# Optimization experiments

Hardware: AMD Instinct MI355X
Metric: run time of the kernel (lower is better)

## Reference

```python
import jax, jax.numpy as jnp
import numpy as np

N, D_IN, D_H, D_A, K = 131072, 768, 128, 32, 64
BN_EPS = 1e-5

def setup_inputs() -> dict:
    key = jax.random.key(0)
    ks = jax.random.split(key, 16)
    def lin(k, fan_in, shape):
        return (jax.random.uniform(k, shape, jnp.float32, -1.0, 1.0) / np.sqrt(fan_in)).astype(jnp.float32)
    return {
        "input": jax.random.normal(ks[0], (1, N, D_IN), jnp.float32),
        # linear: Linear(768,128) + BN(128)
        "W1": lin(ks[1], D_IN, (D_IN, D_H)), "b1": lin(ks[2], D_IN, (D_H,)),
        "g1": jnp.ones((D_H,), jnp.float32), "be1": jnp.zeros((D_H,), jnp.float32),
        # attention: Linear(128,32) + BN(32) + Tanh + Linear(32,1)
        "Watt1": lin(ks[3], D_H, (D_H, D_A)), "batt1": lin(ks[4], D_H, (D_A,)),
        "g2": jnp.ones((D_A,), jnp.float32), "be2": jnp.zeros((D_A,), jnp.float32),
        "Watt2": lin(ks[5], D_A, (D_A, 1)), "batt2": lin(ks[6], D_A, (1,)),
        # Wa ModuleList: three Linear(128,32, bias=False)
        "Wq": lin(ks[7], D_H, (D_H, D_A)),
        "Wk": lin(ks[8], D_H, (D_H, D_A)),
        "Wv": lin(ks[9], D_H, (D_H, D_A)),
        # linear_z: Linear(32*k, 128)
        "Wz": lin(ks[10], D_A * K, (D_A * K, D_H)), "bz": lin(ks[11], D_A * K, (D_H,)),
        # fc: Linear(128, 1)
        "Wf": lin(ks[12], D_H, (D_H, 1)), "bf": lin(ks[13], D_H, (1,)),
    }

def reference(input, W1, b1, g1, be1, Watt1, batt1, g2, be2, Watt2, batt2,
              Wq, Wk, Wv, Wz, bz, Wf, bf):
    k = Wz.shape[0] // D_A  # static
    inv = 1.0 / jnp.sqrt(1.0 + BN_EPS)  # BN eval: running_mean=0, running_var=1
    x = input[0]  # [N, 768]
    x = jax.nn.relu((x @ W1 + b1) * (g1 * inv) + be1)  # [N, 128]
    h = jnp.tanh((x @ Watt1 + batt1) * (g2 * inv) + be2)  # [N, 32]
    A = jax.nn.softmax((h @ Watt2 + batt2)[:, 0], axis=0)  # [N]
    order = jnp.argsort(-A)           # descending sort indices
    A_sorted = A[order]
    zs = x[order[:k]] * jax.nn.softmax(A_sorted[:k])[:, None]  # [k, 128]
    zq, zk_, zv = zs @ Wq, zs @ Wk, zs @ Wv                    # [k, 32] each
    zw = jax.nn.softmax(zq @ zk_.T, axis=1) @ zv               # [k, 32]
    zw = jax.nn.relu(zw.reshape(1, -1) @ Wz + bz)              # [1, 128]
    return zw @ Wf + bf                                        # [1, 1]
```

## Files before the change

### kernel.cpp

```cpp
#include <hip/hip_runtime.h>


#define NN   131072
#define DIN  768
#define DH   128
#define DA   32

using f32x4  = __attribute__((ext_vector_type(4))) float;
using bf16x8 = __attribute__((ext_vector_type(8))) __bf16;

#define WS_S      0
#define WS_PZ4    524288
#define WS_HIST   540672
#define WS_MISC   557056
#define WS_CIDX   557120
#define WS_CS     559168
#define WS_ORDER  561216
#define WS_W      561472
#define WS_ZQ     561728
#define WS_ZK     569920
#define WS_ZV     578112
#define WS_ZW     586304
#define WS_O128   594496
#define WS_W1T    598016

__device__ __forceinline__ int s_bin(float s) {
  int b = (int)((s + 6.0f) * (4096.0f / 12.0f));
  return b < 0 ? 0 : (b > 4095 ? 4095 : b);
}

__device__ __forceinline__ void gl_lds16(const void* g, void* l) {
  __builtin_amdgcn_global_load_lds(
      (const __attribute__((address_space(1))) void*)g,
      (__attribute__((address_space(3))) void*)l, 16, 0, 0);
}

__global__ void k_prep(const float* __restrict__ W1, char* __restrict__ ws) {
  int T = blockIdx.x * 256 + threadIdx.x;
  int u = T & 7, col = (T >> 3) & 127, kc = T >> 10;
  bf16x8 ov;
  #pragma unroll
  for (int j = 0; j < 8; ++j) {
    int k = (u & 3) * 8 + j;
    float v = W1[(size_t)(kc * 32 + k) * 128 + col];
    __bf16 h = (__bf16)v;
    ov[j] = (u < 4) ? h : (__bf16)(v - (float)h);
  }
  char* dst = ws + WS_W1T + (size_t)kc * 16384 + col * 128 + ((u ^ (col & 7)) << 4);
  *(bf16x8*)dst = ov;
}

__global__ __launch_bounds__(256, 2) void k_main(
    const float* __restrict__ inp,
    const float* __restrict__ b1, const float* __restrict__ g1, const float* __restrict__ be1,
    const float* __restrict__ Watt1, const float* __restrict__ batt1,
    const float* __restrict__ g2, const float* __restrict__ be2,
    const float* __restrict__ Watt2, const float* __restrict__ batt2,
    char* __restrict__ ws)
{
  __shared__ __align__(16) char lds[81920];
  float* s_out = (float*)(ws + WS_S);
  float* pz4   = (float*)(ws + WS_PZ4);
  int*   hist  = (int*)(ws + WS_HIST);
  const char* w1t = ws + WS_W1T;

  const int t = threadIdx.x;
  const int l = t & 63;
  const int wid = t >> 6;
  const int wr = wid >> 1, wc = wid & 1;
  const int blockRow = blockIdx.x * 128;
  const float inv = 1.0f / sqrtf(1.0f + 1e-5f);

  char* Ab0 = lds;            char* Ab1 = lds + 16384;
  char* Bb0 = lds + 32768;    char* Bb1 = lds + 49152;
  float* xt  = (float*)lds;
  float* wat = (float*)(lds + 65536);

  for (int i = t; i < DH * DA; i += 256) wat[i] = Watt1[i];

  const int sr = t >> 3;
  const int su = (t & 7) ^ (sr & 7);
  const float* aSrc = inp + (size_t)(blockRow + sr) * DIN + su * 4;
  const char*  bSrc = w1t + t * 16;

  f32x4 acc[4][4];
  #pragma unroll
  for (int i = 0; i < 4; ++i)
    #pragma unroll
    for (int j = 0; j < 4; ++j)
      #pragma unroll
      for (int q = 0; q < 4; ++q) acc[i][j][q] = 0.0f;

#define STAGE(Abuf, Bbuf, kc_) do { \
    _Pragma("unroll") \
    for (int c = 0; c < 4; ++c) \
      gl_lds16(aSrc + (size_t)c * 24576 + (kc_) * 32, (Abuf) + c * 4096 + t * 16); \
    _Pragma("unroll") \
    for (int c = 0; c < 4; ++c) \
      gl_lds16(bSrc + (size_t)(kc_) * 16384 + c * 4096, (Bbuf) + c * 4096 + t * 16); \
  } while (0)

  STAGE(Ab0, Bb0, 0);

  const int kg = l >> 4, r15 = l & 15;
  for (int kc = 0; kc < 24; ++kc) {
    char* A = (kc & 1) ? Ab1 : Ab0;
    char* B = (kc & 1) ? Bb1 : Bb0;
    if (kc < 23) {
      char* An = (kc & 1) ? Ab0 : Ab1;
      char* Bn = (kc & 1) ? Bb0 : Bb1;
      STAGE(An, Bn, kc + 1);
      asm volatile("s_waitcnt vmcnt(8)" ::: "memory");
    } else {
      asm volatile("s_waitcnt vmcnt(0)" ::: "memory");
    }
    __builtin_amdgcn_sched_barrier(0);
    __builtin_amdgcn_s_barrier();
    __builtin_amdgcn_sched_barrier(0);

    bf16x8 ahi[4], alo[4];
    #pragma unroll
    for (int mi = 0; mi < 4; ++mi) {
      int R = wr * 64 + mi * 16 + r15;
      const char* base = A + R * 128; int sw = R & 7;
      f32x4 a0 = *(const f32x4*)(base + (((kg * 2)     ^ sw) << 4));
      f32x4 a1 = *(const f32x4*)(base + (((kg * 2 + 1) ^ sw) << 4));
      #pragma unroll
      for (int j = 0; j < 4; ++j) {
        float x0 = a0[j]; __bf16 h0 = (__bf16)x0; ahi[mi][j]     = h0; alo[mi][j]     = (__bf16)(x0 - (float)h0);
        float x1 = a1[j]; __bf16 h1 = (__bf16)x1; ahi[mi][4 + j] = h1; alo[mi][4 + j] = (__bf16)(x1 - (float)h1);
      }
    }
    #pragma unroll
    for (int ni = 0; ni < 4; ++ni) {
      int C = wc * 64 + ni * 16 + r15;
      const char* cb = B + C * 128; int sw = C & 7;
      bf16x8 bhi = *(const bf16x8*)(cb + ((kg       ^ sw) << 4));
      bf16x8 blo = *(const bf16x8*)(cb + (((4 | kg) ^ sw) << 4));
      #pragma unroll
      for (int mi = 0; mi < 4; ++mi) {
        acc[mi][ni] = __builtin_amdgcn_mfma_f32_16x16x32_bf16(ahi[mi], bhi, acc[mi][ni], 0, 0, 0);
        acc[mi][ni] = __builtin_amdgcn_mfma_f32_16x16x32_bf16(ahi[mi], blo, acc[mi][ni], 0, 0, 0);
        acc[mi][ni] = __builtin_amdgcn_mfma_f32_16x16x32_bf16(alo[mi], bhi, acc[mi][ni], 0, 0, 0);
      }
    }
    __builtin_amdgcn_sched_barrier(0);
    __builtin_amdgcn_s_barrier();
    __builtin_amdgcn_sched_barrier(0);
  }
#undef STAGE

  __syncthreads();
  #pragma unroll
  for (int ni = 0; ni < 4; ++ni) {
    int col = wc * 64 + ni * 16 + r15;
    float b1c = b1[col], s1c = g1[col] * inv, be1c = be1[col];
    #pragma unroll
    for (int mi = 0; mi < 4; ++mi) {
      int rbase = wr * 64 + mi * 16 + ((l >> 4) << 2);
      #pragma unroll
      for (int q = 0; q < 4; ++q) {
        int row = rbase + q;
        float xv = fmaxf((acc[mi][ni][q] + b1c) * s1c + be1c, 0.0f);
        *(float*)((char*)xt + row * 512 + ((col * 4) ^ ((row & 31) << 4))) = xv;
      }
    }
  }
  __syncthreads();
  {
    const int row = t >> 1, ah = t & 1;
    float hacc[16];
    #pragma unroll
    for (int a = 0; a < 16; ++a) hacc[a] = 0.0f;
    const char* xrow = (const char*)xt + row * 512;
    const int rsw = (row & 31) << 4;
    for (int cb = 0; cb < 128; cb += 4) {
      f32x4 xv = *(const f32x4*)(xrow + ((cb * 4) ^ rsw));
      #pragma unroll
      for (int u = 0; u < 4; ++u) {
        const float* wrow = wat + (cb + u) * 32 + ah * 16;
        f32x4 w0 = *(const f32x4*)(wrow);
        f32x4 w1 = *(const f32x4*)(wrow + 4);
        f32x4 w2 = *(const f32x4*)(wrow + 8);
        f32x4 w3 = *(const f32x4*)(wrow + 12);
        float xs = xv[u];
        #pragma unroll
        for (int q = 0; q < 4; ++q) {
          hacc[q]     += xs * w0[q];
          hacc[4 + q] += xs * w1[q];
          hacc[8 + q] += xs * w2[q];
          hacc[12 + q]+= xs * w3[q];
        }
      }
    }
    float partial = 0.0f;
    #pragma unroll
    for (int a = 0; a < 16; ++a) {
      int ai = ah * 16 + a;
      float hv = tanhf((hacc[a] + batt1[ai]) * (g2[ai] * inv) + be2[ai]);
      partial += hv * Watt2[ai];
    }
    partial += __shfl_xor(partial, 1, 64);
    float ev = 0.0f;
    if (ah == 0) {
      float sv = partial + batt2[0];
      s_out[blockRow + row] = sv;
      atomicAdd(&hist[s_bin(sv)], 1);
      ev = expf(sv);
    }
    #pragma unroll
    for (int off = 32; off >= 1; off >>= 1) ev += __shfl_xor(ev, off, 64);
    if (l == 0) pz4[blockIdx.x * 4 + wid] = ev;
  }
}

__global__ void k_reduce(char* __restrict__ ws) {
  float* pz4 = (float*)(ws + WS_PZ4);
  int* hist = (int*)(ws + WS_HIST);
  float* miscf = (float*)(ws + WS_MISC);
  int* misci = (int*)(ws + WS_MISC);
  const int t = threadIdx.x;
  __shared__ float red[256];
  __shared__ int csum[256];
  float z = 0.0f;
  for (int i = t; i < 4096; i += 256) z += pz4[i];
  red[t] = z;
  int c = 0;
  #pragma unroll
  for (int u = 0; u < 16; ++u) c += hist[t * 16 + u];
  csum[t] = c;
  __syncthreads();
  for (int off = 128; off >= 1; off >>= 1) {
    if (t < off) red[t] += red[t + off];
    __syncthreads();
  }
  if (t == 0) {
    miscf[0] = red[0];
    int cum = 0, bstar = 0;
    for (int ch = 255; ch >= 0; --ch) {
      if (cum + csum[ch] >= 64) {
        for (int b = ch * 16 + 15; b >= ch * 16; --b) {
          cum += hist[b];
          if (cum >= 64) { bstar = b; break; }
        }
        break;
      }
      cum += csum[ch];
    }
    misci[3] = bstar;
    misci[2] = 0;
  }
}

__global__ void k_gather(char* __restrict__ ws) {
  const int i = blockIdx.x * 256 + threadIdx.x;
  float* s_out = (float*)(ws + WS_S);
  int* misci = (int*)(ws + WS_MISC);
  int* cidx = (int*)(ws + WS_CIDX);
  float* cs = (float*)(ws + WS_CS);
  float s = s_out[i];
  if (s_bin(s) >= misci[3]) {
    int pos = atomicAdd(&misci[2], 1);
    if (pos < 512) { cidx[pos] = i; cs[pos] = s; }
  }
}

__global__ void k_select(char* __restrict__ ws) {
  const int t = threadIdx.x;
  float* s_out = (float*)(ws + WS_S);
  int* misci = (int*)(ws + WS_MISC);
  float* miscf = (float*)(ws + WS_MISC);
  int* cidx = (int*)(ws + WS_CIDX);
  float* cs = (float*)(ws + WS_CS);
  int* order = (int*)(ws + WS_ORDER);
  float* wsel = (float*)(ws + WS_W);
  __shared__ unsigned long long keys[512];
  __shared__ float aLds[64];
  int cnt = misci[2]; if (cnt > 512) cnt = 512;
  for (int i = t; i < 512; i += 256) {
    unsigned long long kkey = 0xFFFFFFFFFFFFFFFFull;
    if (i < cnt) {
      unsigned u = __float_as_uint(cs[i]);
      u = (u & 0x80000000u) ? ~u : (u | 0x80000000u);
      unsigned du = ~u;
      kkey = ((unsigned long long)du << 32) | (unsigned)cidx[i];
    }
    keys[i] = kkey;
  }
  __syncthreads();
  for (int k = 2; k <= 512; k <<= 1) {
    for (int j = k >> 1; j > 0; j >>= 1) {
      for (int i = t; i < 512; i += 256) {
        int ixj = i ^ j;
        if (ixj > i) {
          bool up = ((i & k) == 0);
          unsigned long long a = keys[i], b2 = keys[ixj];
          if (up ? (a > b2) : (a < b2)) { keys[i] = b2; keys[ixj] = a; }
        }
      }
      __syncthreads();
    }
  }
  float Z = miscf[0];
  if (t < 64) {
    int idx = (int)(keys[t] & 0xFFFFFFFFull);
    order[t] = idx;
    aLds[t] = expf(s_out[idx]) / Z;
  }
  __syncthreads();
  if (t < 64) {
    float m = aLds[0];
    float e = expf(aLds[t] - m);
    float sum = e;
    #pragma unroll
    for (int off = 32; off >= 1; off >>= 1) sum += __shfl_xor(sum, off, 64);
    wsel[t] = e / sum;
  }
}

__global__ void k_zs(const float* __restrict__ inp, const float* __restrict__ W1,
                     const float* __restrict__ b1, const float* __restrict__ g1, const float* __restrict__ be1,
                     const float* __restrict__ Wq, const float* __restrict__ Wk, const float* __restrict__ Wv,
                     char* __restrict__ ws)
{
  const int t = threadIdx.x, b = blockIdx.x;
  int* order = (int*)(ws + WS_ORDER);
  float* wsel = (float*)(ws + WS_W);
  float* zq = (float*)(ws + WS_ZQ);
  float* zk = (float*)(ws + WS_ZK);
  float* zv = (float*)(ws + WS_ZV);
  __shared__ float rowS[768];
  __shared__ float zsS[128];
  const float inv = 1.0f / sqrtf(1.0f + 1e-5f);
  int r = order[b];
  float wgt = wsel[b];
  for (int i = t; i < 768; i += 256) rowS[i] = inp[(size_t)r * 768 + i];
  __syncthreads();
  if (t < 128) {
    float d = 0.0f;
    for (int k = 0; k < 768; ++k) d += rowS[k] * W1[(size_t)k * 128 + t];
    float x = fmaxf((d + b1[t]) * (g1[t] * inv) + be1[t], 0.0f);
    zsS[t] = x * wgt;
  }
  __syncthreads();
  if (t < 96) {
    int which = t >> 5, a = t & 31;
    const float* W = (which == 0) ? Wq : ((which == 1) ? Wk : Wv);
    float d = 0.0f;
    for (int c = 0; c < 128; ++c) d += zsS[c] * W[c * 32 + a];
    float* dst = (which == 0) ? zq : ((which == 1) ? zk : zv);
    dst[b * 32 + a] = d;
  }
}

__global__ void k_attn(char* __restrict__ ws) {
  const int t = threadIdx.x;
  float* zq = (float*)(ws + WS_ZQ);
  float* zk = (float*)(ws + WS_ZK);
  float* zv = (float*)(ws + WS_ZV);
  float* zw = (float*)(ws + WS_ZW);
  __shared__ float q[2048], kk[2048], v[2048], P[4096];
  for (int i = t; i < 2048; i += 256) { q[i] = zq[i]; kk[i] = zk[i]; v[i] = zv[i]; }
  __syncthreads();
  for (int o = t; o < 4096; o += 256) {
    int i = o >> 6, j = o & 63;
    float d = 0.0f;
    for (int a = 0; a < 32; ++a) d += q[i * 32 + a] * kk[j * 32 + a];
    P[o] = d;
  }
  __syncthreads();
  if (t < 64) {
    float m = -1e30f;
    for (int j = 0; j < 64; ++j) m = fmaxf(m, P[t * 64 + j]);
    float sum = 0.0f;
    for (int j = 0; j < 64; ++j) { float e = expf(P[t * 64 + j] - m); P[t * 64 + j] = e; sum += e; }
    float rs = 1.0f / sum;
    for (int j = 0; j < 64; ++j) P[t * 64 + j] *= rs;
  }
  __syncthreads();
  for (int o = t; o < 2048; o += 256) {
    int i = o >> 5, a = o & 31;
    float d = 0.0f;
    for (int j = 0; j < 64; ++j) d += P[i * 64 + j] * v[j * 32 + a];
    zw[o] = d;
  }
}

__global__ void k_wz(const float* __restrict__ Wz, const float* __restrict__ bz, char* __restrict__ ws) {
  const int t = threadIdx.x, j = blockIdx.x;
  float* zw = (float*)(ws + WS_ZW);
  float* o128 = (float*)(ws + WS_O128);
  __shared__ float red[256];
  float p = 0.0f;
  for (int i2 = t; i2 < 2048; i2 += 256) p += zw[i2] * Wz[(size_t)i2 * 128 + j];
  red[t] = p; __syncthreads();
  for (int off = 128; off >= 1; off >>= 1) {
    if (t < off) red[t] += red[t + off];
    __syncthreads();
  }
  if (t == 0) o128[j] = fmaxf(red[0] + bz[j], 0.0f);
}

__global__ void k_final(const float* __restrict__ Wf, const float* __restrict__ bf_,
                        char* __restrict__ ws, float* __restrict__ out) {
  const int t = threadIdx.x;
  float* o128 = (float*)(ws + WS_O128);
  __shared__ float red[128];
  red[t] = o128[t] * Wf[t];
  __syncthreads();
  for (int off = 64; off >= 1; off >>= 1) {
    if (t < off) red[t] += red[t + off];
    __syncthreads();
  }
  if (t == 0) out[0] = red[0] + bf_[0];
}

extern "C" void kernel_launch(void* const* d_in, const int* in_sizes, int n_in,
                              void* d_out, int out_size, void* d_ws, size_t ws_size,
                              hipStream_t stream) {
  const float* inp   = (const float*)d_in[0];
  const float* W1    = (const float*)d_in[1];
  const float* b1    = (const float*)d_in[2];
  const float* g1    = (const float*)d_in[3];
  const float* be1   = (const float*)d_in[4];
  const float* Watt1 = (const float*)d_in[5];
  const float* batt1 = (const float*)d_in[6];
  const float* g2    = (const float*)d_in[7];
  const float* be2   = (const float*)d_in[8];
  const float* Watt2 = (const float*)d_in[9];
  const float* batt2 = (const float*)d_in[10];
  const float* Wq    = (const float*)d_in[11];
  const float* Wk    = (const float*)d_in[12];
  const float* Wv    = (const float*)d_in[13];
  const float* Wz    = (const float*)d_in[14];
  const float* bz    = (const float*)d_in[15];
  const float* Wf    = (const float*)d_in[16];
  const float* bf_   = (const float*)d_in[17];
  char* ws = (char*)d_ws;

  hipMemsetAsync(ws + WS_HIST, 0, 16384 + 64, stream);
  k_prep<<<dim3(96), dim3(256), 0, stream>>>(W1, ws);
  k_main<<<dim3(1024), dim3(256), 0, stream>>>(inp, b1, g1, be1, Watt1, batt1, g2, be2, Watt2, batt2, ws);
  k_reduce<<<dim3(1), dim3(256), 0, stream>>>(ws);
  k_gather<<<dim3(512), dim3(256), 0, stream>>>(ws);
  k_select<<<dim3(1), dim3(256), 0, stream>>>(ws);
  k_zs<<<dim3(64), dim3(256), 0, stream>>>(inp, W1, b1, g1, be1, Wq, Wk, Wv, ws);
  k_attn<<<dim3(1), dim3(256), 0, stream>>>(ws);
  k_wz<<<dim3(128), dim3(256), 0, stream>>>(Wz, bz, ws);
  k_final<<<dim3(1), dim3(128), 0, stream>>>(Wf, bf_, ws, (float*)d_out);
}
```

Before: 287.1 us.

## Read W1 fragments from global, shrink LDS for occupancy 3, fuse tail kernels

The main GEMM kernel stops staging the pre-split W1 tile through LDS and loads B fragments straight from global/L2 into registers. The A input stays double-buffered in LDS. The epilogue processes the 128 rows in two 64-row passes so LDS shrinks from 80KB to 48KB and launch bounds rise to 3 blocks per CU. Smaller changes remove the hipMemset by zeroing the histogram in k_prep, and fold k_final into k_wz with an atomicAdd on the output. The cost is a full vmcnt(0) wait every iteration, which loses overlap between loads and compute, plus extra barriers in the epilogue.

```diff
diff --git a/kernel.cpp b/kernel.cpp
--- a/kernel.cpp
+++ b/kernel.cpp
@@ -10,19 +10,18 @@
 using bf16x8 = __attribute__((ext_vector_type(8))) __bf16;
 
 #define WS_S      0
-#define WS_PZ4    524288
-#define WS_HIST   540672
-#define WS_MISC   557056
-#define WS_CIDX   557120
-#define WS_CS     559168
-#define WS_ORDER  561216
-#define WS_W      561472
-#define WS_ZQ     561728
-#define WS_ZK     569920
-#define WS_ZV     578112
-#define WS_ZW     586304
-#define WS_O128   594496
-#define WS_W1T    598016
+#define WS_PZ8    524288
+#define WS_HIST   557056
+#define WS_MISC   573440
+#define WS_CIDX   573504
+#define WS_CS     575552
+#define WS_ORDER  577600
+#define WS_W      577856
+#define WS_ZQ     578112
+#define WS_ZK     586304
+#define WS_ZV     594496
+#define WS_ZW     602688
+#define WS_W1T    610944
 
 __device__ __forceinline__ int s_bin(float s) {
   int b = (int)((s + 6.0f) * (4096.0f / 12.0f));
@@ -37,6 +36,7 @@
 
 __global__ void k_prep(const float* __restrict__ W1, char* __restrict__ ws) {
   int T = blockIdx.x * 256 + threadIdx.x;
+  if (T < 4112) ((int*)(ws + WS_HIST))[T] = 0;
   int u = T & 7, col = (T >> 3) & 127, kc = T >> 10;
   bf16x8 ov;
   #pragma unroll
@@ -46,11 +46,10 @@
     __bf16 h = (__bf16)v;
     ov[j] = (u < 4) ? h : (__bf16)(v - (float)h);
   }
-  char* dst = ws + WS_W1T + (size_t)kc * 16384 + col * 128 + ((u ^ (col & 7)) << 4);
-  *(bf16x8*)dst = ov;
-}
-
-__global__ __launch_bounds__(256, 2) void k_main(
+  *(bf16x8*)(ws + WS_W1T + (size_t)kc * 16384 + col * 128 + u * 16) = ov;
+}
+
+__global__ __launch_bounds__(256, 3) void k_main(
     const float* __restrict__ inp,
     const float* __restrict__ b1, const float* __restrict__ g1, const float* __restrict__ be1,
     const float* __restrict__ Watt1, const float* __restrict__ batt1,
@@ -58,9 +57,9 @@
     const float* __restrict__ Watt2, const float* __restrict__ batt2,
     char* __restrict__ ws)
 {
-  __shared__ __align__(16) char lds[81920];
+  __shared__ __align__(16) char lds[49152];
   float* s_out = (float*)(ws + WS_S);
-  float* pz4   = (float*)(ws + WS_PZ4);
+  float* pz8   = (float*)(ws + WS_PZ8);
   int*   hist  = (int*)(ws + WS_HIST);
   const char* w1t = ws + WS_W1T;
 
@@ -71,17 +70,20 @@
   const int blockRow = blockIdx.x * 128;
   const float inv = 1.0f / sqrtf(1.0f + 1e-5f);
 
-  char* Ab0 = lds;            char* Ab1 = lds + 16384;
-  char* Bb0 = lds + 32768;    char* Bb1 = lds + 49152;
-  float* xt  = (float*)lds;
-  float* wat = (float*)(lds + 65536);
-
-  for (int i = t; i < DH * DA; i += 256) wat[i] = Watt1[i];
+  char* Ab0 = lds;
+  char* Ab1 = lds + 16384;
+  char* xh  = lds;
+  float* wat = (float*)(lds + 32768);
 
   const int sr = t >> 3;
   const int su = (t & 7) ^ (sr & 7);
   const float* aSrc = inp + (size_t)(blockRow + sr) * DIN + su * 4;
-  const char*  bSrc = w1t + t * 16;
+  #pragma unroll
+  for (int c = 0; c < 4; ++c)
+    gl_lds16(Watt1 + c * 1024 + t * 4, (char*)wat + c * 4096 + t * 16);
+  #pragma unroll
+  for (int c = 0; c < 4; ++c)
+    gl_lds16(aSrc + (size_t)c * 24576, Ab0 + c * 4096 + t * 16);
 
   f32x4 acc[4][4];
   #pragma unroll
@@ -91,29 +93,11 @@
       #pragma unroll
       for (int q = 0; q < 4; ++q) acc[i][j][q] = 0.0f;
 
-#define STAGE(Abuf, Bbuf, kc_) do { \
-    _Pragma("unroll") \
-    for (int c = 0; c < 4; ++c) \
-      gl_lds16(aSrc + (size_t)c * 24576 + (kc_) * 32, (Abuf) + c * 4096 + t * 16); \
-    _Pragma("unroll") \
-    for (int c = 0; c < 4; ++c) \
-      gl_lds16(bSrc + (size_t)(kc_) * 16384 + c * 4096, (Bbuf) + c * 4096 + t * 16); \
-  } while (0)
-
-  STAGE(Ab0, Bb0, 0);
-
   const int kg = l >> 4, r15 = l & 15;
   for (int kc = 0; kc < 24; ++kc) {
-    char* A = (kc & 1) ? Ab1 : Ab0;
-    char* B = (kc & 1) ? Bb1 : Bb0;
-    if (kc < 23) {
-      char* An = (kc & 1) ? Ab0 : Ab1;
-      char* Bn = (kc & 1) ? Bb0 : Bb1;
-      STAGE(An, Bn, kc + 1);
-      asm volatile("s_waitcnt vmcnt(8)" ::: "memory");
-    } else {
-      asm volatile("s_waitcnt vmcnt(0)" ::: "memory");
-    }
+    const char* A = (kc & 1) ? Ab1 : Ab0;
+    char* An = (kc & 1) ? Ab0 : Ab1;
+    asm volatile("s_waitcnt vmcnt(0)" ::: "memory");
     __builtin_amdgcn_sched_barrier(0);
     __builtin_amdgcn_s_barrier();
     __builtin_amdgcn_sched_barrier(0);
@@ -127,95 +111,102 @@
       f32x4 a1 = *(const f32x4*)(base + (((kg * 2 + 1) ^ sw) << 4));
       #pragma unroll
       for (int j = 0; j < 4; ++j) {
-        float x0 = a0[j]; __bf16 h0 = (__bf16)x0; ahi[mi][j]     = h0; alo[mi][j]     = (__bf16)(x0 - (float)h0);
-        float x1 = a1[j]; __bf16 h1 = (__bf16)x1; ahi[mi][4 + j] = h1; alo[mi][4 + j] = (__bf16)(x1 - (float)h1);
-      }
-    }
+        float x0 = a0[j]; __bf16 h0 = (__bf16)x0;
+        ahi[mi][j] = h0;     alo[mi][j] = (__bf16)(x0 - (float)h0);
+        float x1 = a1[j]; __bf16 h1 = (__bf16)x1;
+        ahi[mi][4+j] = h1;   alo[mi][4+j] = (__bf16)(x1 - (float)h1);
+      }
+    }
+    __builtin_amdgcn_sched_barrier(0);
+    bf16x8 bhi[4], blo[4];
     #pragma unroll
     for (int ni = 0; ni < 4; ++ni) {
-      int C = wc * 64 + ni * 16 + r15;
-      const char* cb = B + C * 128; int sw = C & 7;
-      bf16x8 bhi = *(const bf16x8*)(cb + ((kg       ^ sw) << 4));
-      bf16x8 blo = *(const bf16x8*)(cb + (((4 | kg) ^ sw) << 4));
+      const char* bb = w1t + (size_t)kc * 16384 + (wc * 64 + ni * 16 + r15) * 128;
+      bhi[ni] = *(const bf16x8*)(bb + (kg << 4));
+      blo[ni] = *(const bf16x8*)(bb + 64 + (kg << 4));
+    }
+    __builtin_amdgcn_sched_barrier(0);
+    if (kc < 23) {
+      #pragma unroll
+      for (int c = 0; c < 4; ++c)
+        gl_lds16(aSrc + (size_t)c * 24576 + (kc + 1) * 32, An + c * 4096 + t * 16);
+    }
+    __builtin_amdgcn_sched_barrier(0);
+    #pragma unroll
+    for (int ni = 0; ni < 4; ++ni)
       #pragma unroll
       for (int mi = 0; mi < 4; ++mi) {
-        acc[mi][ni] = __builtin_amdgcn_mfma_f32_16x16x32_bf16(ahi[mi], bhi, acc[mi][ni], 0, 0, 0);
-        acc[mi][ni] = __builtin_amdgcn_mfma_f32_16x16x32_bf16(ahi[mi], blo, acc[mi][ni], 0, 0, 0);
-        acc[mi][ni] = __builtin_amdgcn_mfma_f32_16x16x32_bf16(alo[mi], bhi, acc[mi][ni], 0, 0, 0);
-      }
-    }
-    __builtin_amdgcn_sched_barrier(0);
-    __builtin_amdgcn_s_barrier();
-    __builtin_amdgcn_sched_barrier(0);
-  }
-#undef STAGE
-
-  __syncthreads();
-  #pragma unroll
-  for (int ni = 0; ni < 4; ++ni) {
-    int col = wc * 64 + ni * 16 + r15;
-    float b1c = b1[col], s1c = g1[col] * inv, be1c = be1[col];
-    #pragma unroll
-    for (int mi = 0; mi < 4; ++mi) {
-      int rbase = wr * 64 + mi * 16 + ((l >> 4) << 2);
-      #pragma unroll
-      for (int q = 0; q < 4; ++q) {
-        int row = rbase + q;
-        float xv = fmaxf((acc[mi][ni][q] + b1c) * s1c + be1c, 0.0f);
-        *(float*)((char*)xt + row * 512 + ((col * 4) ^ ((row & 31) << 4))) = xv;
-      }
-    }
-  }
-  __syncthreads();
-  {
-    const int row = t >> 1, ah = t & 1;
-    float hacc[16];
-    #pragma unroll
-    for (int a = 0; a < 16; ++a) hacc[a] = 0.0f;
-    const char* xrow = (const char*)xt + row * 512;
-    const int rsw = (row & 31) << 4;
+        acc[mi][ni] = __builtin_amdgcn_mfma_f32_16x16x32_bf16(ahi[mi], bhi[ni], acc[mi][ni], 0, 0, 0);
+        acc[mi][ni] = __builtin_amdgcn_mfma_f32_16x16x32_bf16(ahi[mi], blo[ni], acc[mi][ni], 0, 0, 0);
+        acc[mi][ni] = __builtin_amdgcn_mfma_f32_16x16x32_bf16(alo[mi], bhi[ni], acc[mi][ni], 0, 0, 0);
+      }
+  }
+
+  __syncthreads();
+  const int row = t >> 2, q4 = t & 3;
+  const int rsw = (row & 31) << 4;
+  for (int pass = 0; pass < 2; ++pass) {
+    if (wr == pass) {
+      #pragma unroll
+      for (int ni = 0; ni < 4; ++ni) {
+        int col = wc * 64 + ni * 16 + r15;
+        float b1c = b1[col], s1c = g1[col] * inv, be1c = be1[col];
+        #pragma unroll
+        for (int mi = 0; mi < 4; ++mi) {
+          #pragma unroll
+          for (int q = 0; q < 4; ++q) {
+            int rloc = mi * 16 + kg * 4 + q;
+            float xv = fmaxf((acc[mi][ni][q] + b1c) * s1c + be1c, 0.0f);
+            *(float*)(xh + rloc * 512 + ((col * 4) ^ ((rloc & 31) << 4))) = xv;
+          }
+        }
+      }
+    }
+    __syncthreads();
+    float hacc[8];
+    #pragma unroll
+    for (int a = 0; a < 8; ++a) hacc[a] = 0.0f;
+    const char* xrow = xh + row * 512;
     for (int cb = 0; cb < 128; cb += 4) {
       f32x4 xv = *(const f32x4*)(xrow + ((cb * 4) ^ rsw));
       #pragma unroll
       for (int u = 0; u < 4; ++u) {
-        const float* wrow = wat + (cb + u) * 32 + ah * 16;
+        const float* wrow = wat + (cb + u) * 32 + q4 * 8;
         f32x4 w0 = *(const f32x4*)(wrow);
         f32x4 w1 = *(const f32x4*)(wrow + 4);
-        f32x4 w2 = *(const f32x4*)(wrow + 8);
-        f32x4 w3 = *(const f32x4*)(wrow + 12);
         float xs = xv[u];
         #pragma unroll
         for (int q = 0; q < 4; ++q) {
           hacc[q]     += xs * w0[q];
           hacc[4 + q] += xs * w1[q];
-          hacc[8 + q] += xs * w2[q];
-          hacc[12 + q]+= xs * w3[q];
         }
       }
     }
     float partial = 0.0f;
     #pragma unroll
-    for (int a = 0; a < 16; ++a) {
-      int ai = ah * 16 + a;
+    for (int a = 0; a < 8; ++a) {
+      int ai = q4 * 8 + a;
       float hv = tanhf((hacc[a] + batt1[ai]) * (g2[ai] * inv) + be2[ai]);
       partial += hv * Watt2[ai];
     }
     partial += __shfl_xor(partial, 1, 64);
+    partial += __shfl_xor(partial, 2, 64);
     float ev = 0.0f;
-    if (ah == 0) {
+    if (q4 == 0) {
       float sv = partial + batt2[0];
-      s_out[blockRow + row] = sv;
+      s_out[blockRow + pass * 64 + row] = sv;
       atomicAdd(&hist[s_bin(sv)], 1);
       ev = expf(sv);
     }
     #pragma unroll
     for (int off = 32; off >= 1; off >>= 1) ev += __shfl_xor(ev, off, 64);
-    if (l == 0) pz4[blockIdx.x * 4 + wid] = ev;
+    if (l == 0) pz8[blockIdx.x * 8 + pass * 4 + wid] = ev;
+    __syncthreads();
   }
 }
 
 __global__ void k_reduce(char* __restrict__ ws) {
-  float* pz4 = (float*)(ws + WS_PZ4);
+  float* pz8 = (float*)(ws + WS_PZ8);
   int* hist = (int*)(ws + WS_HIST);
   float* miscf = (float*)(ws + WS_MISC);
   int* misci = (int*)(ws + WS_MISC);
@@ -223,7 +214,7 @@
   __shared__ float red[256];
   __shared__ int csum[256];
   float z = 0.0f;
-  for (int i = t; i < 4096; i += 256) z += pz4[i];
+  for (int i = t; i < 8192; i += 256) z += pz8[i];
   red[t] = z;
   int c = 0;
   #pragma unroll
@@ -353,8 +344,9 @@
   }
 }
 
-__global__ void k_attn(char* __restrict__ ws) {
+__global__ void k_attn(char* __restrict__ ws, float* __restrict__ out) {
   const int t = threadIdx.x;
+  if (t == 0) out[0] = 0.0f;
   float* zq = (float*)(ws + WS_ZQ);
   float* zk = (float*)(ws + WS_ZK);
   float* zv = (float*)(ws + WS_ZV);
@@ -386,10 +378,11 @@
   }
 }
 
-__global__ void k_wz(const float* __restrict__ Wz, const float* __restrict__ bz, char* __restrict__ ws) {
+__global__ void k_wz(const float* __restrict__ Wz, const float* __restrict__ bz,
+                     const float* __restrict__ Wf, const float* __restrict__ bf_,
+                     char* __restrict__ ws, float* __restrict__ out) {
   const int t = threadIdx.x, j = blockIdx.x;
   float* zw = (float*)(ws + WS_ZW);
-  float* o128 = (float*)(ws + WS_O128);
   __shared__ float red[256];
   float p = 0.0f;
   for (int i2 = t; i2 < 2048; i2 += 256) p += zw[i2] * Wz[(size_t)i2 * 128 + j];
@@ -398,21 +391,11 @@
     if (t < off) red[t] += red[t + off];
     __syncthreads();
   }
-  if (t == 0) o128[j] = fmaxf(red[0] + bz[j], 0.0f);
-}
-
-__global__ void k_final(const float* __restrict__ Wf, const float* __restrict__ bf_,
-                        char* __restrict__ ws, float* __restrict__ out) {
-  const int t = threadIdx.x;
-  float* o128 = (float*)(ws + WS_O128);
-  __shared__ float red[128];
-  red[t] = o128[t] * Wf[t];
-  __syncthreads();
-  for (int off = 64; off >= 1; off >>= 1) {
-    if (t < off) red[t] += red[t + off];
-    __syncthreads();
-  }
-  if (t == 0) out[0] = red[0] + bf_[0];
+  if (t == 0) {
+    float o = fmaxf(red[0] + bz[j], 0.0f);
+    float contrib = o * Wf[j] + (j == 0 ? bf_[0] : 0.0f);
+    atomicAdd(out, contrib);
+  }
 }
 
 extern "C" void kernel_launch(void* const* d_in, const int* in_sizes, int n_in,
@@ -438,14 +421,12 @@
   const float* bf_   = (const float*)d_in[17];
   char* ws = (char*)d_ws;
 
-  hipMemsetAsync(ws + WS_HIST, 0, 16384 + 64, stream);
   k_prep<<<dim3(96), dim3(256), 0, stream>>>(W1, ws);
   k_main<<<dim3(1024), dim3(256), 0, stream>>>(inp, b1, g1, be1, Watt1, batt1, g2, be2, Watt2, batt2, ws);
   k_reduce<<<dim3(1), dim3(256), 0, stream>>>(ws);
   k_gather<<<dim3(512), dim3(256), 0, stream>>>(ws);
   k_select<<<dim3(1), dim3(256), 0, stream>>>(ws);
   k_zs<<<dim3(64), dim3(256), 0, stream>>>(inp, W1, b1, g1, be1, Wq, Wk, Wv, ws);
-  k_attn<<<dim3(1), dim3(256), 0, stream>>>(ws);
-  k_wz<<<dim3(128), dim3(256), 0, stream>>>(Wz, bz, ws);
-  k_final<<<dim3(1), dim3(128), 0, stream>>>(Wf, bf_, ws, (float*)d_out);
-}
+  k_attn<<<dim3(1), dim3(256), 0, stream>>>(ws, (float*)d_out);
+  k_wz<<<dim3(128), dim3(256), 0, stream>>>(Wz, bz, Wf, bf_, ws, (float*)d_out);
+}
```

Result: slower. 352.4 us (+22.7%).
